# Optimization experiments

Hardware: AMD Instinct MI355X
Metric: run time of the kernel (lower is better)

Reference implementation:

```python
import jax, jax.numpy as jnp
import numpy as np

B, T, ENC, DEC = 32, 2000, 1024, 1024
ATTN, OUT, H, C, KS = 512, 1024, 4, 64, 50
KLEN = 2 * KS + 1
SCALING = 1.0
PH = OUT // H  # per-head output dim


def setup_inputs() -> dict:
    key = jax.random.key(0)
    ks = jax.random.split(key, 12)
    s = 0.02
    return {
        "enc_states": jax.random.normal(ks[0], (B, T, ENC), jnp.float32),
        "enc_len": jax.random.randint(ks[1], (B,), T // 2, T + 1, jnp.int32),
        "dec_states": jax.random.normal(ks[2], (B, DEC), jnp.float32),
        "Wenc": jax.random.normal(ks[3], (H, ATTN, ENC), jnp.float32) * s,
        "benc": jnp.zeros((H, ATTN), jnp.float32),
        "Wdec": jax.random.normal(ks[4], (H, ATTN, DEC), jnp.float32) * s,
        "bdec": jnp.zeros((H, ATTN), jnp.float32),
        "wattn": jax.random.normal(ks[5], (H, ATTN), jnp.float32) * s,
        "Wconv": jax.random.normal(ks[6], (H * C, 1, KLEN), jnp.float32) * s,
        "Wloc": jax.random.normal(ks[7], (H, ATTN, C), jnp.float32) * s,
        "bloc": jnp.zeros((H, ATTN), jnp.float32),
        "Wout": jax.random.normal(ks[8], (H, PH, ENC), jnp.float32) * s,
        "bout": jnp.zeros((H, PH), jnp.float32),
    }


def reference(enc_states, enc_len, dec_states, Wenc, benc, Wdec, bdec, wattn,
              Wconv, Wloc, bloc, Wout, bout):
    dt = enc_states.dtype
    mask = jnp.arange(T)[None, :] < enc_len[:, None]            # [B,T] bool
    fmask = mask.astype(dt)
    # initial prev_attn: uniform over valid frames (first decoding step)
    prev_attn = fmask / enc_len[:, None].astype(dt)             # [B,T]
    # location conv for all heads at once: [B,1,T] x [H*C,1,K] -> [B,H*C,T]
    conv = jax.lax.conv_general_dilated(
        prev_attn[:, None, :], Wconv, window_strides=(1,),
        padding=[(KS, KS)], dimension_numbers=("NCH", "OIH", "NCH"))
    conv = conv.reshape(B, H, C, T)
    loc = jnp.einsum("bhct,hac->hbta", conv, Wloc) + bloc[:, None, None, :]
    enc_h = jnp.einsum("bte,hae->hbta", enc_states, Wenc) + benc[:, None, None, :]
    dec_h = jnp.einsum("bd,had->hba", dec_states, Wdec) + bdec[:, None, :]
    # additive attention scores per head: [H,B,T]
    scores = jnp.einsum("hbta,ha->hbt",
                        jnp.tanh(enc_h + dec_h[:, :, None, :] + loc), wattn)
    scores = jnp.where(mask[None], scores * SCALING, -jnp.inf)
    attn = jax.nn.softmax(scores, axis=-1)                      # [H,B,T]
    ctx = jnp.einsum("hbt,bte->hbe", attn, enc_states)          # [H,B,ENC]
    out = jnp.einsum("hbe,hoe->hbo", ctx, Wout) + bout[:, None, :]
    context = jnp.transpose(out, (1, 0, 2)).reshape(B, OUT)     # cat heads dim=1
    attn_weight = attn.mean(axis=0)                             # [B,T]
    return context, attn_weight
```

## Files before the change

kernel.cpp:

```cpp
#include <hip/hip_runtime.h>
#include <hip/hip_bf16.h>
#include <cstdint>

#define NB 32
#define NT 2000
#define TP 2048
#define NENC 1024
#define NDEC 1024
#define NATTN 512
#define NHEAD 4
#define NH 2048
#define NC 64
#define NKS 50
#define NKLEN 101
#define NPH 256
#define NPROF 101
#define NTS 16
#define TCH 125

typedef __attribute__((ext_vector_type(8))) short bf16x8;
typedef __attribute__((ext_vector_type(4))) float f32x4;
typedef __attribute__((ext_vector_type(8))) unsigned short u16x8;

__device__ __forceinline__ void gload_lds16(const void* g, void* l) {
    __builtin_amdgcn_global_load_lds((__attribute__((address_space(1))) void*)(g),
                                     (__attribute__((address_space(3))) void*)(l), 16, 0, 0);
}

__device__ __forceinline__ unsigned short f2bf(float f) {
    unsigned u = __float_as_uint(f);
    return (unsigned short)((u + 0x7fffu + ((u >> 16) & 1u)) >> 16);
}

__device__ __forceinline__ float bf2f(unsigned short u) {
    return __uint_as_float((unsigned)u << 16);
}

__device__ __forceinline__ int prof_of(int t, int len) {
    if (t < NKS) return t;
    if (t < len - NKS) return NKS;
    if (t < len) return NKS + 1 + (t - (len - NKS));
    return NKS;
}

__device__ __forceinline__ float4 f4add3(float4 a, float4 b, float4 c) {
    return make_float4(a.x + b.x + c.x, a.y + b.y + c.y, a.z + b.z + c.z, a.w + b.w + c.w);
}
__device__ __forceinline__ float4 f4fma(float s, float4 a, float4 acc) {
    return make_float4(fmaf(s, a.x, acc.x), fmaf(s, a.y, acc.y),
                       fmaf(s, a.z, acc.z), fmaf(s, a.w, acc.w));
}
__device__ __forceinline__ float f4dot(float4 a, float4 b) {
    return fmaf(a.x, b.x, fmaf(a.y, b.y, fmaf(a.z, b.z, a.w * b.w)));
}

__global__ void k_convert2(const float* __restrict__ srcA, unsigned short* __restrict__ dstA, int n8A,
                           const float* __restrict__ srcB, unsigned short* __restrict__ dstB, int n8B) {
    int stride = gridDim.x * blockDim.x;
    int total = n8A + n8B;
    for (int i = blockIdx.x * blockDim.x + threadIdx.x; i < total; i += stride) {
        const float* src; unsigned short* dst; int j;
        if (i < n8A) { src = srcA; dst = dstA; j = i; }
        else         { src = srcB; dst = dstB; j = i - n8A; }
        const float4* s = (const float4*)(src) + (size_t)j * 2;
        float4 x = s[0], y = s[1];
        u16x8 o;
        o[0] = f2bf(x.x); o[1] = f2bf(x.y); o[2] = f2bf(x.z); o[3] = f2bf(x.w);
        o[4] = f2bf(y.x); o[5] = f2bf(y.y); o[6] = f2bf(y.z); o[7] = f2bf(y.w);
        *((u16x8*)dst + j) = o;
    }
}

__global__ void k_prep(const float* __restrict__ Wconv, float* __restrict__ wcum,
                       const float* __restrict__ Wloc, float* __restrict__ wlocT,
                       const float* __restrict__ dec, const float* __restrict__ Wdec,
                       const float* __restrict__ bdec, float* __restrict__ dech) {
    int blk = blockIdx.x;
    int tid = threadIdx.x;
    if (blk == 0) {
        float c = 0.f;
        wcum[tid * 102] = 0.f;
        for (int k = 0; k < NKLEN; ++k) {
            c += Wconv[tid * NKLEN + k];
            wcum[tid * 102 + k + 1] = c;
        }
    } else if (blk <= 64) {
        int c = blk - 1;
        for (int n = tid; n < NH; n += 256)
            wlocT[c * NH + n] = Wloc[(size_t)n * NC + c];
    } else {
        int idx = blk - 65;
        int h = idx >> 5, b = idx & 31;
        __shared__ float dl[NDEC];
        for (int r = 0; r < 4; ++r) dl[tid + r * 256] = dec[b * NDEC + tid + r * 256];
        __syncthreads();
        for (int a2 = 0; a2 < 2; ++a2) {
            int a = tid + a2 * 256;
            const float4* wr = (const float4*)&Wdec[((size_t)(h * NATTN + a)) * NDEC];
            float acc = 0.f;
            for (int e4 = 0; e4 < NDEC / 4; ++e4) {
                float4 w4 = wr[e4];
                acc += w4.x * dl[e4 * 4] + w4.y * dl[e4 * 4 + 1] + w4.z * dl[e4 * 4 + 2] + w4.w * dl[e4 * 4 + 3];
            }
            dech[(h * NB + b) * NATTN + a] = acc + bdec[h * NATTN + a];
        }
    }
}

__global__ void k_addprof(const float* __restrict__ wcum, const float* __restrict__ dech,
                          const float* __restrict__ benc, const float* __restrict__ bloc,
                          const float* __restrict__ wlocT, const int* __restrict__ enc_len,
                          float* __restrict__ addp) {
    int p0 = blockIdx.x * 8, b = blockIdx.y;
    int len = enc_len[b];
    __shared__ float convp[8][256];
    int tid = threadIdx.x;
    float invl = 1.f / (float)len;
#pragma unroll
    for (int pp = 0; pp < 8; ++pp) {
        int p = min(p0 + pp, NPROF - 1);
        int kmin, kmax;
        if (p < NKS)       { kmin = NKS - p; kmax = min(NKLEN, len - p + NKS); }
        else if (p == NKS) { kmin = 0;       kmax = NKLEN; }
        else               { kmin = 0;       kmax = 151 - p; }
        if (kmax < kmin) kmax = kmin;
        convp[pp][tid] = (wcum[tid * 102 + kmax] - wcum[tid * 102 + kmin]) * invl;
    }
    __syncthreads();
    int h0 = tid >> 7, h1 = 2 + h0;
    int n40 = tid, n41 = 256 + tid;
    const float4* dech4 = (const float4*)dech;
    const float4* benc4 = (const float4*)benc;
    const float4* bloc4 = (const float4*)bloc;
    float4 base0 = f4add3(dech4[(h0 * NB + b) * 128 + (tid & 127)], benc4[n40], bloc4[n40]);
    float4 base1 = f4add3(dech4[(h1 * NB + b) * 128 + (tid & 127)], benc4[n41], bloc4[n41]);
    float4 acc[8][2];
#pragma unroll
    for (int pp = 0; pp < 8; ++pp) { acc[pp][0] = base0; acc[pp][1] = base1; }
    const float4* wT4 = (const float4*)wlocT;
#pragma unroll 2
    for (int c = 0; c < NC; ++c) {
        float4 w0 = wT4[c * 512 + n40];
        float4 w1 = wT4[c * 512 + n41];
#pragma unroll
        for (int pp = 0; pp < 8; ++pp) {
            acc[pp][0] = f4fma(convp[pp][h0 * 64 + c], w0, acc[pp][0]);
            acc[pp][1] = f4fma(convp[pp][h1 * 64 + c], w1, acc[pp][1]);
        }
    }
    float4* addp4 = (float4*)addp;
#pragma unroll
    for (int pp = 0; pp < 8; ++pp) {
        int p = p0 + pp;
        if (p < NPROF) {
            addp4[((size_t)(b * NPROF + p)) * 512 + n40] = acc[pp][0];
            addp4[((size_t)(b * NPROF + p)) * 512 + n41] = acc[pp][1];
        }
    }
}

__global__ __launch_bounds__(256, 3) void k_gemm(
        const unsigned short* __restrict__ encbf, const unsigned short* __restrict__ wencbf,
        const float* __restrict__ addp, const float* __restrict__ wattn,
        const int* __restrict__ enc_len, float* __restrict__ scores) {
    extern __shared__ char smem[];
    int bid = blockIdx.x;
    int L = (bid & 7) * 1024 + (bid >> 3);
    int nt = L & 15, ty = (L >> 4) & 15, b = L >> 8;
    int n0 = nt * 128, t0 = ty * 128;
    int len = enc_len[b];
    if (t0 >= len) return;
    int tid = threadIdx.x, lane = tid & 63, w = tid >> 6;
    int wr = w >> 1, wc = w & 1;
    int ro = lane & 15, g4 = lane >> 4;

    int lrow = lane >> 2;
    int csrc = ((lane & 3) ^ ((lane >> 3) & 3)) * 8;
    const unsigned short* aB = encbf + (size_t)b * NT * NENC;
    int rA[2], rB[2];
#pragma unroll
    for (int g = 0; g < 2; ++g) { int t = t0 + g * 64 + w * 16 + lrow; rA[g] = t < NT ? t : NT - 1; }
#pragma unroll
    for (int g = 0; g < 2; ++g) rB[g] = n0 + g * 64 + w * 16 + lrow;

    auto STAGE = [&](int q, int kt) {
        char* base = smem + q * 16384;
        int k0 = kt * 32 + csrc;
#pragma unroll
        for (int g = 0; g < 2; ++g)
            gload_lds16(aB + (size_t)rA[g] * NENC + k0, base + g * 4096 + w * 1024);
#pragma unroll
        for (int g = 0; g < 2; ++g)
            gload_lds16(wencbf + (size_t)rB[g] * NENC + k0, base + 8192 + g * 4096 + w * 1024);
    };

    f32x4 acc[4][4] = {};
    int swb = (g4 ^ ((ro >> 1) & 3)) * 16;
    int rdA = (wr * 64 + ro) * 64 + swb;
    int rdB = 8192 + (wc * 64 + ro) * 64 + swb;

    STAGE(0, 0);
    __syncthreads();
#pragma unroll 2
    for (int kt = 0; kt < 32; ++kt) {
        int q = kt & 1;
        if (kt < 31) STAGE(q ^ 1, kt + 1);
        const char* base = smem + q * 16384;
        bf16x8 A[4], Bf[4];
#pragma unroll
        for (int m = 0; m < 4; ++m) A[m] = *(const bf16x8*)(base + rdA + m * 1024);
#pragma unroll
        for (int n = 0; n < 4; ++n) Bf[n] = *(const bf16x8*)(base + rdB + n * 1024);
        __builtin_amdgcn_s_setprio(1);
#pragma unroll
        for (int m = 0; m < 4; ++m) {
            acc[m][0] = __builtin_amdgcn_mfma_f32_16x16x32_bf16(A[m], Bf[0], acc[m][0], 0, 0, 0);
            acc[m][1] = __builtin_amdgcn_mfma_f32_16x16x32_bf16(A[m], Bf[1], acc[m][1], 0, 0, 0);
            acc[m][2] = __builtin_amdgcn_mfma_f32_16x16x32_bf16(A[m], Bf[2], acc[m][2], 0, 0, 0);
            acc[m][3] = __builtin_amdgcn_mfma_f32_16x16x32_bf16(A[m], Bf[3], acc[m][3], 0, 0, 0);
        }
        __builtin_amdgcn_s_setprio(0);
        __syncthreads();
    }

    int h = n0 >> 9;
    float wat[4];
#pragma unroll
    for (int n = 0; n < 4; ++n) wat[n] = wattn[n0 + wc * 64 + n * 16 + ro];
    const float* addb = addp + (size_t)b * NPROF * NH + n0 + wc * 64 + ro;
    float* sr = scores + ((size_t)(h * NB + b)) * TP;
#pragma unroll
    for (int m = 0; m < 4; ++m) {
#pragma unroll
        for (int e = 0; e < 4; ++e) {
            int t = t0 + wr * 64 + m * 16 + g4 * 4 + e;
            int tc = t < NT ? t : NT - 1;
            const float* arow = addb + (size_t)prof_of(tc, len) * NH;
            float s = 0.f;
#pragma unroll
            for (int n = 0; n < 4; ++n) {
                float v = acc[m][n][e] + arow[n * 16];
                v = fminf(fmaxf(v, -15.f), 15.f);
                float e2 = __expf(2.f * v);
                s += ((e2 - 1.f) / (e2 + 1.f)) * wat[n];
            }
            s += __shfl_xor(s, 1); s += __shfl_xor(s, 2);
            s += __shfl_xor(s, 4); s += __shfl_xor(s, 8);
            if (ro == 0 && t < NT) atomicAdd(&sr[t], s);
        }
    }
}

__global__ void k_softmax(const float* __restrict__ scores, const int* __restrict__ enc_len,
                          float* __restrict__ attn, float* __restrict__ out) {
    int h = blockIdx.x >> 5, b = blockIdx.x & 31;
    int len = enc_len[b];
    int tid = threadIdx.x;
    const float* row = scores + ((size_t)(h * NB + b)) * TP;
    __shared__ float red[4];
    float m = -1e30f;
    for (int t = tid; t < len; t += 256) m = fmaxf(m, row[t]);
    for (int d = 32; d; d >>= 1) m = fmaxf(m, __shfl_xor(m, d));
    if ((tid & 63) == 0) red[tid >> 6] = m;
    __syncthreads();
    m = fmaxf(fmaxf(red[0], red[1]), fmaxf(red[2], red[3]));
    __syncthreads();
    float z = 0.f;
    for (int t = tid; t < len; t += 256) z += __expf(row[t] - m);
    for (int d = 32; d; d >>= 1) z += __shfl_xor(z, d);
    if ((tid & 63) == 0) red[tid >> 6] = z;
    __syncthreads();
    z = red[0] + red[1] + red[2] + red[3];
    float inv = 1.f / z;
    float* ow = out + NB * 1024 + b * NT;
    for (int t = tid; t < NT; t += 256) {
        float av = (t < len) ? __expf(row[t] - m) * inv : 0.f;
        attn[((size_t)(h * NB + b)) * NT + t] = av;
        atomicAdd(&ow[t], 0.25f * av);
    }
}

__global__ void k_ctx(const unsigned short* __restrict__ encbf, const float* __restrict__ attn,
                      const int* __restrict__ enc_len, float* __restrict__ ctxp) {
    int ec = blockIdx.x, ts = blockIdx.y, b = blockIdx.z;
    int tid = threadIdx.x;
    __shared__ float attnL[NHEAD][TCH];
    int t0 = ts * TCH;
    for (int i = tid; i < NHEAD * TCH; i += 256) {
        int hh = i / TCH, tt = i - hh * TCH;
        attnL[hh][tt] = attn[((size_t)(hh * NB + b)) * NT + t0 + tt];
    }
    __syncthreads();
    int len = enc_len[b];
    int t1 = min(t0 + TCH, len);
    int e0 = ec * 512 + tid * 2;
    const unsigned* erow = (const unsigned*)(encbf + (size_t)b * NT * NENC);
    float a0x = 0.f, a0y = 0.f, a1x = 0.f, a1y = 0.f;
    float a2x = 0.f, a2y = 0.f, a3x = 0.f, a3y = 0.f;
    int t = t0;
    for (; t + 2 <= t1; t += 2) {
        unsigned pv0 = erow[((size_t)t * NENC + e0) >> 1];
        unsigned pv1 = erow[((size_t)(t + 1) * NENC + e0) >> 1];
        int tt = t - t0;
        float ex0 = bf2f((unsigned short)(pv0 & 0xffff));
        float ey0 = bf2f((unsigned short)(pv0 >> 16));
        float w00 = attnL[0][tt], w10 = attnL[1][tt], w20 = attnL[2][tt], w30 = attnL[3][tt];
        a0x = fmaf(w00, ex0, a0x); a0y = fmaf(w00, ey0, a0y);
        a1x = fmaf(w10, ex0, a1x); a1y = fmaf(w10, ey0, a1y);
        a2x = fmaf(w20, ex0, a2x); a2y = fmaf(w20, ey0, a2y);
        a3x = fmaf(w30, ex0, a3x); a3y = fmaf(w30, ey0, a3y);
        float ex1 = bf2f((unsigned short)(pv1 & 0xffff));
        float ey1 = bf2f((unsigned short)(pv1 >> 16));
        float w01 = attnL[0][tt + 1], w11 = attnL[1][tt + 1], w21 = attnL[2][tt + 1], w31 = attnL[3][tt + 1];
        a0x = fmaf(w01, ex1, a0x); a0y = fmaf(w01, ey1, a0y);
        a1x = fmaf(w11, ex1, a1x); a1y = fmaf(w11, ey1, a1y);
        a2x = fmaf(w21, ex1, a2x); a2y = fmaf(w21, ey1, a2y);
        a3x = fmaf(w31, ex1, a3x); a3y = fmaf(w31, ey1, a3y);
    }
    for (; t < t1; ++t) {
        unsigned pv = erow[((size_t)t * NENC + e0) >> 1];
        float ex = bf2f((unsigned short)(pv & 0xffff));
        float ey = bf2f((unsigned short)(pv >> 16));
        int tt = t - t0;
        float w0 = attnL[0][tt], w1 = attnL[1][tt], w2 = attnL[2][tt], w3 = attnL[3][tt];
        a0x = fmaf(w0, ex, a0x); a0y = fmaf(w0, ey, a0y);
        a1x = fmaf(w1, ex, a1x); a1y = fmaf(w1, ey, a1y);
        a2x = fmaf(w2, ex, a2x); a2y = fmaf(w2, ey, a2y);
        a3x = fmaf(w3, ex, a3x); a3y = fmaf(w3, ey, a3y);
    }
    float2* c0 = (float2*)&ctxp[(((size_t)ts * NHEAD + 0) * NB + b) * NENC + e0];
    float2* c1 = (float2*)&ctxp[(((size_t)ts * NHEAD + 1) * NB + b) * NENC + e0];
    float2* c2 = (float2*)&ctxp[(((size_t)ts * NHEAD + 2) * NB + b) * NENC + e0];
    float2* c3 = (float2*)&ctxp[(((size_t)ts * NHEAD + 3) * NB + b) * NENC + e0];
    *c0 = make_float2(a0x, a0y);
    *c1 = make_float2(a1x, a1y);
    *c2 = make_float2(a2x, a2y);
    *c3 = make_float2(a3x, a3y);
}

__global__ void k_out(const float* __restrict__ ctxp, const float* __restrict__ Wout,
                      const float* __restrict__ bout, float* __restrict__ out) {
    int b = blockIdx.x, h = blockIdx.y;
    int tid = threadIdx.x;
    __shared__ __align__(16) float ctxL[NENC];
    for (int r = 0; r < 4; ++r) {
        int e = tid + r * 256;
        float s = 0.f;
#pragma unroll
        for (int s4 = 0; s4 < NTS; ++s4) s += ctxp[(((size_t)s4 * NHEAD + h) * NB + b) * NENC + e];
        ctxL[e] = s;
    }
    __syncthreads();
    int o = tid;
    const float4* wrow = (const float4*)&Wout[((size_t)(h * NPH + o)) * NENC];
    const float4* cl4 = (const float4*)ctxL;
    float s0 = 0.f, s1 = 0.f, s2 = 0.f, s3 = 0.f;
    for (int i = 0; i < NENC / 16; ++i) {
        s0 += f4dot(wrow[4 * i + 0], cl4[4 * i + 0]);
        s1 += f4dot(wrow[4 * i + 1], cl4[4 * i + 1]);
        s2 += f4dot(wrow[4 * i + 2], cl4[4 * i + 2]);
        s3 += f4dot(wrow[4 * i + 3], cl4[4 * i + 3]);
    }
    out[b * 1024 + h * NPH + o] = bout[h * NPH + o] + ((s0 + s1) + (s2 + s3));
}

extern "C" void kernel_launch(void* const* d_in, const int* in_sizes, int n_in,
                              void* d_out, int out_size, void* d_ws, size_t ws_size,
                              hipStream_t stream) {
    const float* enc   = (const float*)d_in[0];
    const int*   elen  = (const int*)d_in[1];
    const float* dec   = (const float*)d_in[2];
    const float* Wenc  = (const float*)d_in[3];
    const float* benc  = (const float*)d_in[4];
    const float* Wdec  = (const float*)d_in[5];
    const float* bdec  = (const float*)d_in[6];
    const float* wattn = (const float*)d_in[7];
    const float* Wconv = (const float*)d_in[8];
    const float* Wloc  = (const float*)d_in[9];
    const float* bloc  = (const float*)d_in[10];
    const float* Wout  = (const float*)d_in[11];
    const float* bout  = (const float*)d_in[12];
    float* out = (float*)d_out;

    char* ws = (char*)d_ws;
    size_t off = 0;
    auto alloc = [&](size_t bytes) { size_t o = off; off += (bytes + 255) & ~(size_t)255; return o; };
    unsigned short* encbf  = (unsigned short*)(ws + alloc((size_t)NB * NT * NENC * 2));
    unsigned short* wencbf = (unsigned short*)(ws + alloc((size_t)NH * NENC * 2));
    float* wcum  = (float*)(ws + alloc((size_t)256 * 102 * 4));
    float* wlocT = (float*)(ws + alloc((size_t)NC * NH * 4));
    float* dech  = (float*)(ws + alloc((size_t)NHEAD * NB * NATTN * 4));
    float* addp  = (float*)(ws + alloc((size_t)NB * NPROF * NH * 4));
    float* scor  = (float*)(ws + alloc((size_t)NHEAD * NB * TP * 4));
    float* attn  = (float*)(ws + alloc((size_t)NHEAD * NB * NT * 4));
    float* ctxp  = (float*)(ws + alloc((size_t)NTS * NHEAD * NB * NENC * 4));
    if (off > ws_size) return;

    hipFuncSetAttribute((const void*)k_gemm, hipFuncAttributeMaxDynamicSharedMemorySize, 32768);

    k_convert2<<<2048, 256, 0, stream>>>(enc, encbf, NB * NT * NENC / 8,
                                         Wenc, wencbf, NH * NENC / 8);
    k_prep<<<193, 256, 0, stream>>>(Wconv, wcum, Wloc, wlocT, dec, Wdec, bdec, dech);
    k_addprof<<<dim3((NPROF + 7) / 8, NB), 256, 0, stream>>>(wcum, dech, benc, bloc, wlocT, elen, addp);
    hipMemsetAsync(scor, 0, (size_t)NHEAD * NB * TP * 4, stream);
    hipMemsetAsync(out + NB * 1024, 0, (size_t)NB * NT * 4, stream);
    k_gemm<<<8192, 256, 32768, stream>>>(encbf, wencbf, addp, wattn, elen, scor);
    k_softmax<<<NHEAD * NB, 256, 0, stream>>>(scor, elen, attn, out);
    k_ctx<<<dim3(2, NTS, NB), 256, 0, stream>>>(encbf, attn, elen, ctxp);
    k_out<<<dim3(NB, NHEAD), 256, 0, stream>>>(ctxp, Wout, bout, out);
}
```

Baseline: 517.2 us.

## Load GEMM B operand directly into registers, bypassing LDS staging

The Wenc (B) tile is no longer staged through shared memory. Each wave loads its B fragments straight from global memory into registers, double-buffered in registers across an explicitly unrolled pair of k-steps, and LDS now holds only the A tile (16 KB instead of 32 KB). This is meant to cut LDS traffic and footprint, which may allow more resident blocks. In exchange, each wave issues redundant global loads of B (the two row-warps read the same B columns), and the extra B registers may add register pressure.

```diff
diff --git a/kernel.cpp b/kernel.cpp
--- a/kernel.cpp
+++ b/kernel.cpp
@@ -177,51 +177,57 @@
     int lrow = lane >> 2;
     int csrc = ((lane & 3) ^ ((lane >> 3) & 3)) * 8;
     const unsigned short* aB = encbf + (size_t)b * NT * NENC;
-    int rA[2], rB[2];
+    int rA[2];
 #pragma unroll
     for (int g = 0; g < 2; ++g) { int t = t0 + g * 64 + w * 16 + lrow; rA[g] = t < NT ? t : NT - 1; }
-#pragma unroll
-    for (int g = 0; g < 2; ++g) rB[g] = n0 + g * 64 + w * 16 + lrow;
-
-    auto STAGE = [&](int q, int kt) {
-        char* base = smem + q * 16384;
+
+    auto STAGE_A = [&](int q, int kt) {
+        char* base = smem + q * 8192;
         int k0 = kt * 32 + csrc;
 #pragma unroll
         for (int g = 0; g < 2; ++g)
             gload_lds16(aB + (size_t)rA[g] * NENC + k0, base + g * 4096 + w * 1024);
-#pragma unroll
-        for (int g = 0; g < 2; ++g)
-            gload_lds16(wencbf + (size_t)rB[g] * NENC + k0, base + 8192 + g * 4096 + w * 1024);
     };
+
+    const unsigned short* bBase = wencbf + (size_t)(n0 + wc * 64 + ro) * NENC + g4 * 8;
+    bf16x8 B0[4], B1[4];
+#define LOADB(BF, KT) { _Pragma("unroll") \
+    for (int n = 0; n < 4; ++n) BF[n] = *(const bf16x8*)(bBase + (size_t)n * 16 * NENC + (KT) * 32); }
 
     f32x4 acc[4][4] = {};
     int swb = (g4 ^ ((ro >> 1) & 3)) * 16;
     int rdA = (wr * 64 + ro) * 64 + swb;
-    int rdB = 8192 + (wc * 64 + ro) * 64 + swb;
-
-    STAGE(0, 0);
-    __syncthreads();
-#pragma unroll 2
-    for (int kt = 0; kt < 32; ++kt) {
-        int q = kt & 1;
-        if (kt < 31) STAGE(q ^ 1, kt + 1);
-        const char* base = smem + q * 16384;
-        bf16x8 A[4], Bf[4];
-#pragma unroll
-        for (int m = 0; m < 4; ++m) A[m] = *(const bf16x8*)(base + rdA + m * 1024);
-#pragma unroll
-        for (int n = 0; n < 4; ++n) Bf[n] = *(const bf16x8*)(base + rdB + n * 1024);
-        __builtin_amdgcn_s_setprio(1);
-#pragma unroll
-        for (int m = 0; m < 4; ++m) {
-            acc[m][0] = __builtin_amdgcn_mfma_f32_16x16x32_bf16(A[m], Bf[0], acc[m][0], 0, 0, 0);
-            acc[m][1] = __builtin_amdgcn_mfma_f32_16x16x32_bf16(A[m], Bf[1], acc[m][1], 0, 0, 0);
-            acc[m][2] = __builtin_amdgcn_mfma_f32_16x16x32_bf16(A[m], Bf[2], acc[m][2], 0, 0, 0);
-            acc[m][3] = __builtin_amdgcn_mfma_f32_16x16x32_bf16(A[m], Bf[3], acc[m][3], 0, 0, 0);
-        }
-        __builtin_amdgcn_s_setprio(0);
+
+#define COMPUTE(BASE, BF) { \
+    const char* base_ = (BASE); \
+    bf16x8 A[4]; \
+    _Pragma("unroll") \
+    for (int m = 0; m < 4; ++m) A[m] = *(const bf16x8*)(base_ + rdA + m * 1024); \
+    __builtin_amdgcn_s_setprio(1); \
+    _Pragma("unroll") \
+    for (int m = 0; m < 4; ++m) { \
+        acc[m][0] = __builtin_amdgcn_mfma_f32_16x16x32_bf16(A[m], BF[0], acc[m][0], 0, 0, 0); \
+        acc[m][1] = __builtin_amdgcn_mfma_f32_16x16x32_bf16(A[m], BF[1], acc[m][1], 0, 0, 0); \
+        acc[m][2] = __builtin_amdgcn_mfma_f32_16x16x32_bf16(A[m], BF[2], acc[m][2], 0, 0, 0); \
+        acc[m][3] = __builtin_amdgcn_mfma_f32_16x16x32_bf16(A[m], BF[3], acc[m][3], 0, 0, 0); } \
+    __builtin_amdgcn_s_setprio(0); }
+
+    STAGE_A(0, 0);
+    LOADB(B0, 0);
+    __syncthreads();
+#pragma unroll 1
+    for (int kp = 0; kp < 16; ++kp) {
+        int kt1 = 2 * kp + 1;
+        STAGE_A(1, kt1);
+        LOADB(B1, kt1);
+        COMPUTE(smem, B0);
         __syncthreads();
-    }
+        if (kp < 15) { STAGE_A(0, kt1 + 1); LOADB(B0, kt1 + 1); }
+        COMPUTE(smem + 8192, B1);
+        __syncthreads();
+    }
+#undef COMPUTE
+#undef LOADB
 
     int h = n0 >> 9;
     float wat[4];
@@ -396,7 +402,7 @@
     float* ctxp  = (float*)(ws + alloc((size_t)NTS * NHEAD * NB * NENC * 4));
     if (off > ws_size) return;
 
-    hipFuncSetAttribute((const void*)k_gemm, hipFuncAttributeMaxDynamicSharedMemorySize, 32768);
+    hipFuncSetAttribute((const void*)k_gemm, hipFuncAttributeMaxDynamicSharedMemorySize, 16384);
 
     k_convert2<<<2048, 256, 0, stream>>>(enc, encbf, NB * NT * NENC / 8,
                                          Wenc, wencbf, NH * NENC / 8);
@@ -404,7 +410,7 @@
     k_addprof<<<dim3((NPROF + 7) / 8, NB), 256, 0, stream>>>(wcum, dech, benc, bloc, wlocT, elen, addp);
     hipMemsetAsync(scor, 0, (size_t)NHEAD * NB * TP * 4, stream);
     hipMemsetAsync(out + NB * 1024, 0, (size_t)NB * NT * 4, stream);
-    k_gemm<<<8192, 256, 32768, stream>>>(encbf, wencbf, addp, wattn, elen, scor);
+    k_gemm<<<8192, 256, 16384, stream>>>(encbf, wencbf, addp, wattn, elen, scor);
     k_softmax<<<NHEAD * NB, 256, 0, stream>>>(scor, elen, attn, out);
     k_ctx<<<dim3(2, NTS, NB), 256, 0, stream>>>(encbf, attn, elen, ctxp);
     k_out<<<dim3(NB, NHEAD), 256, 0, stream>>>(ctxp, Wout, bout, out);
```

Result: slower. 712.1 us (+37.7%).
